# Performance work log

Hardware: AMD Instinct MI355X
Metric: run time of the kernel (lower is better)

## Reference

```python
import jax, jax.numpy as jnp
import numpy as np

D_MODEL = 1024
NUM_HEADS = 16
HEAD_DIM = D_MODEL // NUM_HEADS


def setup_inputs() -> dict:
    key = jax.random.key(0)
    ks = jax.random.split(key, 10)
    B, SQ, SK = 2, 2048, 2048
    scale = 1.0 / np.sqrt(D_MODEL)
    inp = {
        "x1": jax.random.normal(ks[0], (B, SQ, D_MODEL), jnp.float32),
        "x2": jax.random.normal(ks[1], (B, SK, D_MODEL), jnp.float32),
        "Wq": jax.random.normal(ks[2], (D_MODEL, D_MODEL), jnp.float32) * scale,
        "bq": jnp.zeros((D_MODEL,), jnp.float32),
        "Wk": jax.random.normal(ks[3], (D_MODEL, D_MODEL), jnp.float32) * scale,
        "bk": jnp.zeros((D_MODEL,), jnp.float32),
        "Wv": jax.random.normal(ks[4], (D_MODEL, D_MODEL), jnp.float32) * scale,
        "bv": jnp.zeros((D_MODEL,), jnp.float32),
        "Wo": jax.random.normal(ks[5], (D_MODEL, D_MODEL), jnp.float32) * scale,
        "bo": jnp.zeros((D_MODEL,), jnp.float32),
    }
    return inp


def reference(x1, x2, Wq, bq, Wk, bk, Wv, bv, Wo, bo):
    B, SQ, _ = x1.shape
    SK = x2.shape[1]
    # projections, then split into heads: [B, H, S, Dh]
    def split_heads(t, S):
        return t.reshape(B, S, NUM_HEADS, HEAD_DIM).transpose(0, 2, 1, 3)
    Q = split_heads(x1 @ Wq + bq, SQ)
    K = split_heads(x2 @ Wk + bk, SK)
    V = split_heads(x2 @ Wv + bv, SK)
    # note: original scales by 1/head_dim**0.5
    scores = jnp.einsum("bhqd,bhkd->bhqk", Q, K) / jnp.sqrt(
        jnp.asarray(HEAD_DIM, Q.dtype))
    attn = jax.nn.softmax(scores, axis=-1)
    ctx = jnp.einsum("bhqk,bhkd->bhqd", attn, V)
    ctx = ctx.transpose(0, 2, 1, 3).reshape(B, SQ, D_MODEL)
    return ctx @ Wo + bo
```

## Files before the change

kernel.cpp:

```cpp
#include <hip/hip_runtime.h>
#include <stdint.h>


typedef unsigned short u16b;
typedef __attribute__((ext_vector_type(4))) short short4v;
typedef __attribute__((ext_vector_type(8))) short short8v;
typedef __attribute__((ext_vector_type(4))) float float4v;
typedef __attribute__((ext_vector_type(2))) unsigned int uint2v;

#if __has_builtin(__builtin_amdgcn_exp2f)
__device__ __forceinline__ float exp2_fast(float x){ return __builtin_amdgcn_exp2f(x); }
#else
__device__ __forceinline__ float exp2_fast(float x){ return exp2f(x); }
#endif

__device__ __forceinline__ float bf2f(u16b u) {
  union { unsigned int i; float f; } v; v.i = ((unsigned int)u) << 16; return v.f;
}
__device__ __forceinline__ u16b f2bf(float f) {
  union { float f; unsigned int i; } v; v.f = f;
  return (u16b)((v.i + 0x7fffu + ((v.i >> 16) & 1u)) >> 16);
}
__device__ __forceinline__ void gl_lds16(const u16b* g, u16b* l) {
  __builtin_amdgcn_global_load_lds(
      (const __attribute__((address_space(1))) void*)g,
      (__attribute__((address_space(3))) void*)l, 16, 0, 0);
}

__global__ __launch_bounds__(256) void cvt2_bf16(
    const float* __restrict__ s0, const float* __restrict__ s1,
    u16b* __restrict__ d0, u16b* __restrict__ d1, int n4) {
  const float* src = blockIdx.y ? s1 : s0;
  u16b* dst = blockIdx.y ? d1 : d0;
  int i = blockIdx.x * blockDim.x + threadIdx.x;
  int stride = gridDim.x * blockDim.x;
  for (; i < n4; i += stride) {
    float4v v = ((const float4v*)src)[i];
    short4v o;
    o[0]=(short)f2bf(v[0]); o[1]=(short)f2bf(v[1]);
    o[2]=(short)f2bf(v[2]); o[3]=(short)f2bf(v[3]);
    ((short4v*)dst)[i] = o;
  }
}

__global__ __launch_bounds__(256) void transposeW(
    const float* __restrict__ W0, const float* __restrict__ W1,
    const float* __restrict__ W2, const float* __restrict__ W3,
    u16b* __restrict__ out) {
  __shared__ u16b tile[32][33];
  const int z = blockIdx.z;
  const float* src = (z==0) ? W0 : (z==1) ? W1 : (z==2) ? W2 : W3;
  u16b* dst = out + (size_t)z * (1024*1024);
  const int x = threadIdx.x, y = threadIdx.y;
  const int bx = blockIdx.x * 32, by = blockIdx.y * 32;
#pragma unroll
  for (int j=0;j<4;++j)
    tile[y*4+j][x] = f2bf(src[(size_t)(by + y*4+j)*1024 + bx + x]);
  __syncthreads();
#pragma unroll
  for (int j=0;j<4;++j)
    dst[(size_t)(bx + y*4+j)*1024 + by + x] = tile[x][y*4+j];
}

template<int BN, int OM>
__device__ __forceinline__ void gemm_core(
    const u16b* __restrict__ A, const u16b* __restrict__ Bt,
    const float* __restrict__ bias, void* __restrict__ Cv,
    int N, int K, int bm, int bn) {
  constexpr int NT = BN / 32;
  __shared__ __align__(16) u16b As[128*32];
  __shared__ __align__(16) u16b Bs[BN*32];
  const int tid = threadIdx.x;
  const int lane = tid & 63, wave = tid >> 6;
  const int wm = wave >> 1, wn = wave & 1;
  const int l15 = lane & 15, l4 = lane >> 4;
  float4v acc[4][NT];
#pragma unroll
  for (int i=0;i<4;++i)
#pragma unroll
    for (int j=0;j<NT;++j) acc[i][j] = (float4v){0.f,0.f,0.f,0.f};

  const int swz = (l15 >> 1) & 3;

  for (int k0 = 0; k0 < K; k0 += 32) {
    __syncthreads();
    {
      int row = tid >> 2, seg = tid & 3;
      int segg0 = seg ^ ((row >> 1) & 3);
      int row2 = row + 64;
      int segg1 = seg ^ ((row2 >> 1) & 3);
      gl_lds16(&A[(size_t)(bm+row )*K + k0 + segg0*8], &As[tid*8]);
      gl_lds16(&A[(size_t)(bm+row2)*K + k0 + segg1*8], &As[(tid+256)*8]);
      gl_lds16(&Bt[(size_t)(bn+row )*K + k0 + segg0*8], &Bs[tid*8]);
      if (BN == 128)
        gl_lds16(&Bt[(size_t)(bn+row2)*K + k0 + segg1*8], &Bs[(tid+256)*8]);
    }
    __syncthreads();
    short8v af[4], bf[NT];
#pragma unroll
    for (int mt=0;mt<4;++mt)
      af[mt] = *(const short8v*)&As[(wm*64+mt*16+l15)*32 + ((l4 ^ swz)*8)];
#pragma unroll
    for (int nt=0;nt<NT;++nt)
      bf[nt] = *(const short8v*)&Bs[(wn*(BN/2)+nt*16+l15)*32 + ((l4 ^ swz)*8)];
#pragma unroll
    for (int mt=0;mt<4;++mt)
#pragma unroll
      for (int nt=0;nt<NT;++nt)
        acc[mt][nt] = __builtin_amdgcn_mfma_f32_16x16x32_bf16(af[mt], bf[nt], acc[mt][nt], 0, 0, 0);
  }

#pragma unroll
  for (int nt=0;nt<NT;++nt) {
    int col = bn + wn*(BN/2) + nt*16 + l15;
    float bb = bias[col];
#pragma unroll
    for (int mt=0;mt<4;++mt) {
      int row0 = bm + wm*64 + mt*16 + l4*4;
      if (OM == 2) {
        int bloc = row0 >> 11, kv0 = row0 & 2047;
        uint2v dw;
        dw[0] = (unsigned)f2bf(acc[mt][nt][0] + bb) | ((unsigned)f2bf(acc[mt][nt][1] + bb) << 16);
        dw[1] = (unsigned)f2bf(acc[mt][nt][2] + bb) | ((unsigned)f2bf(acc[mt][nt][3] + bb) << 16);
        *(uint2v*)((u16b*)Cv + ((size_t)(bloc*1024 + col))*2048 + kv0) = dw;
      } else {
#pragma unroll
        for (int r=0;r<4;++r) {
          float v = acc[mt][nt][r] + bb;
          if (OM == 1) ((float*)Cv)[(size_t)(row0+r)*N + col] = v;
          else         ((u16b*)Cv)[(size_t)(row0+r)*N + col] = f2bf(v);
        }
      }
    }
  }
}

__global__ __launch_bounds__(256) void gemm_qkv(
    const u16b* __restrict__ x1b, const u16b* __restrict__ x2b,
    const u16b* __restrict__ WT, const float* __restrict__ bq,
    const float* __restrict__ bk, const float* __restrict__ bv,
    u16b* __restrict__ out) {
  const int z = blockIdx.z;
  const u16b* A = (z == 0) ? x1b : x2b;
  const u16b* Bt = WT + (size_t)z * (1024*1024);
  u16b* C = out + (size_t)z * (4u*1024*1024);
  if (z == 2)
    gemm_core<128,2>(A, Bt, bv, C, 1024, 1024, blockIdx.y*128, blockIdx.x*128);
  else
    gemm_core<128,0>(A, Bt, (z==0)?bq:bk, C, 1024, 1024, blockIdx.y*128, blockIdx.x*128);
}

__global__ __launch_bounds__(256) void gemm_out(
    const u16b* __restrict__ A, const u16b* __restrict__ Bt,
    const float* __restrict__ bias, float* __restrict__ C) {
  gemm_core<64,1>(A, Bt, bias, C, 1024, 1024, blockIdx.y*128, blockIdx.x*64);
}

__global__ __launch_bounds__(256) void attn128(
    const u16b* __restrict__ Q, const u16b* __restrict__ Kg,
    const u16b* __restrict__ Vt, u16b* __restrict__ O) {
  __shared__ __align__(16) u16b Ks[128*64];
  __shared__ __align__(16) u16b Vs[64*128];
  __shared__ __align__(16) u16b Ps[4*2*16*72];
  const int tid = threadIdx.x;
  const int lane = tid & 63, wave = tid >> 6;
  const int l15 = lane & 15, l4 = lane >> 4;
  const int h = blockIdx.y, b = blockIdx.z;
  const int q0 = blockIdx.x * 128;
  const size_t seqbase = (size_t)b * 2048;
  const int colh = h * 64;
  const int vtbase = (b*16 + h) * 64;
  u16b* Pw = Ps + wave * 2304;

  const float qscale = 0.125f * 1.4426950408889634f;
  short8v qf[2][2];
#pragma unroll
  for (int g=0; g<2; ++g) {
    size_t qrow = seqbase + q0 + wave*32 + g*16 + l15;
#pragma unroll
    for (int ks=0; ks<2; ++ks) {
      short8v raw = *(const short8v*)&Q[qrow*1024 + colh + ks*32 + l4*8];
      short8v s;
#pragma unroll
      for (int i=0;i<8;++i) s[i] = (short)f2bf(bf2f((u16b)raw[i]) * qscale);
      qf[g][ks] = s;
    }
  }

  float lpart[2] = {0.f, 0.f};
  float4v oacc[2][4];
#pragma unroll
  for (int g=0; g<2; ++g)
#pragma unroll
    for (int nb=0; nb<4; ++nb) oacc[g][nb] = (float4v){0.f,0.f,0.f,0.f};

  for (int kt = 0; kt < 16; ++kt) {
    const size_t kvbase = seqbase + (size_t)kt*128;
    __syncthreads();
#pragma unroll
    for (int j=0; j<4; ++j) {
      int idx = j*256 + tid;
      {
        int row = idx >> 3, seg = idx & 7;
        gl_lds16(&Kg[(kvbase+row)*1024 + colh + ((seg ^ (row & 7))*8)], &Ks[idx*8]);
      }
      {
        int row = idx >> 4, seg = idx & 15;
        gl_lds16(&Vt[(size_t)(vtbase+row)*2048 + (size_t)kt*128 + ((seg ^ (row & 15))*8)],
                 &Vs[idx*8]);
      }
    }
    __syncthreads();

    float4v sacc[2][8];
#pragma unroll
    for (int g=0; g<2; ++g)
#pragma unroll
      for (int nb=0; nb<8; ++nb) sacc[g][nb] = (float4v){0.f,0.f,0.f,0.f};
#pragma unroll
    for (int nb=0; nb<8; ++nb)
#pragma unroll
      for (int ks=0; ks<2; ++ks) {
        short8v kf = *(const short8v*)&Ks[(nb*16+l15)*64 + (((ks*4+l4) ^ (l15 & 7))*8)];
        sacc[0][nb] = __builtin_amdgcn_mfma_f32_16x16x32_bf16(kf, qf[0][ks], sacc[0][nb], 0, 0, 0);
        sacc[1][nb] = __builtin_amdgcn_mfma_f32_16x16x32_bf16(kf, qf[1][ks], sacc[1][nb], 0, 0, 0);
      }

#pragma unroll
    for (int h2=0; h2<2; ++h2) {
#pragma unroll
      for (int g=0; g<2; ++g) {
        float ls = 0.f;
#pragma unroll
        for (int nbl=0; nbl<4; ++nbl) {
          const float4v s4 = sacc[g][h2*4 + nbl];
          unsigned int u0 = __float_as_uint(exp2_fast(s4[0]));
          unsigned int u1 = __float_as_uint(exp2_fast(s4[1]));
          unsigned int u2 = __float_as_uint(exp2_fast(s4[2]));
          unsigned int u3 = __float_as_uint(exp2_fast(s4[3]));
          ls += __uint_as_float(u0 & 0xFFFF0000u) + __uint_as_float(u1 & 0xFFFF0000u)
              + __uint_as_float(u2 & 0xFFFF0000u) + __uint_as_float(u3 & 0xFFFF0000u);
          uint2v dw;
          dw[0] = (u0 >> 16) | (u1 & 0xFFFF0000u);
          dw[1] = (u2 >> 16) | (u3 & 0xFFFF0000u);
          *(uint2v*)&Pw[g*1152 + l15*72 + nbl*16 + l4*4] = dw;
        }
        lpart[g] += ls;
      }
      __asm__ __volatile__("s_waitcnt lgkmcnt(0)" ::: "memory");

#pragma unroll
      for (int ks2=0; ks2<2; ++ks2) {
        short8v pf0 = *(const short8v*)&Pw[       l15*72 + ks2*32 + l4*8];
        short8v pf1 = *(const short8v*)&Pw[1152 + l15*72 + ks2*32 + l4*8];
#pragma unroll
        for (int nb=0; nb<4; ++nb) {
          int cc = (h2*8 + ks2*4 + l4) ^ l15;
          short8v vf = *(const short8v*)&Vs[(nb*16+l15)*128 + cc*8];
          oacc[0][nb] = __builtin_amdgcn_mfma_f32_16x16x32_bf16(pf0, vf, oacc[0][nb], 0, 0, 0);
          oacc[1][nb] = __builtin_amdgcn_mfma_f32_16x16x32_bf16(pf1, vf, oacc[1][nb], 0, 0, 0);
        }
      }
    }
  }

#pragma unroll
  for (int g=0; g<2; ++g) {
    float l = lpart[g];
    l += __shfl_xor(l, 16);
    l += __shfl_xor(l, 32);
#pragma unroll
    for (int r=0; r<4; ++r) {
      float ld = __shfl(l, (lane & 48) | (l4*4 + r), 64);
      float inv = 1.0f / ld;
      size_t row = seqbase + q0 + wave*32 + g*16 + l4*4 + r;
#pragma unroll
      for (int nb=0; nb<4; ++nb)
        O[row*1024 + colh + nb*16 + l15] = f2bf(oacc[g][nb][r] * inv);
    }
  }
}

extern "C" void kernel_launch(void* const* d_in, const int* in_sizes, int n_in,
                              void* d_out, int out_size, void* d_ws, size_t ws_size,
                              hipStream_t stream) {
  const float* x1 = (const float*)d_in[0];
  const float* x2 = (const float*)d_in[1];
  const float* Wq = (const float*)d_in[2];
  const float* bq = (const float*)d_in[3];
  const float* Wk = (const float*)d_in[4];
  const float* bk = (const float*)d_in[5];
  const float* Wv = (const float*)d_in[6];
  const float* bv = (const float*)d_in[7];
  const float* Wo = (const float*)d_in[8];
  const float* bo = (const float*)d_in[9];
  (void)in_sizes; (void)n_in; (void)out_size; (void)ws_size;

  u16b* ws = (u16b*)d_ws;
  const size_t Mi = 1024*1024;
  u16b* WT  = ws;
  u16b* WoT = ws + 3*Mi;
  u16b* x1b = ws + 4*Mi;
  u16b* x2b = ws + 8*Mi;
  u16b* QKV = ws + 12*Mi;
  u16b* Qb  = QKV;
  u16b* Kb  = QKV + 4*Mi;
  u16b* Vtb = QKV + 8*Mi;
  u16b* Cx  = x1b;

  cvt2_bf16<<<dim3(1024,2), 256, 0, stream>>>(x1, x2, x1b, x2b, (int)Mi);
  transposeW<<<dim3(32,32,4), dim3(32,8,1), 0, stream>>>(Wq, Wk, Wv, Wo, WT);

  gemm_qkv<<<dim3(8,32,3), 256, 0, stream>>>(x1b, x2b, WT, bq, bk, bv, QKV);

  attn128<<<dim3(16,16,2), 256, 0, stream>>>(Qb, Kb, Vtb, Cx);

  gemm_out<<<dim3(16,32), 256, 0, stream>>>(Cx, WoT, bo, (float*)d_out);
}
```

Measured before the change: 231.0 us.

## Halve attention query tile, compute row sums via MFMA, restructure V projection as transposed GEMM

The attention kernel now processes 64 query rows per block instead of 128, doubling the grid to raise occupancy and parallelism. The block index is ordered batch-head first, so consecutive blocks of one query tile cover different heads. Softmax row sums are accumulated with an extra MFMA against a ones vector instead of scalar adds and shuffles. The P buffer uses an XOR swizzle in place of padding. The V projection is computed as W^T·x^T with a row bias, producing a [1024 x 4096] transposed layout directly through the generic store path instead of a special packed store. The trade-off is that K/V tiles are reloaded twice as often per query row, and the V-projection stores become scalar bf16 writes.

```diff
diff --git a/kernel.cpp b/kernel.cpp
--- a/kernel.cpp
+++ b/kernel.cpp
@@ -62,14 +62,13 @@
     dst[(size_t)(bx + y*4+j)*1024 + by + x] = tile[x][y*4+j];
 }
 
-template<int BN, int OM>
+template<int BN, bool OUT_F32, bool BIAS_ROW>
 __device__ __forceinline__ void gemm_core(
+    u16b* __restrict__ As, u16b* __restrict__ Bs,
     const u16b* __restrict__ A, const u16b* __restrict__ Bt,
     const float* __restrict__ bias, void* __restrict__ Cv,
     int N, int K, int bm, int bn) {
   constexpr int NT = BN / 32;
-  __shared__ __align__(16) u16b As[128*32];
-  __shared__ __align__(16) u16b Bs[BN*32];
   const int tid = threadIdx.x;
   const int lane = tid & 63, wave = tid >> 6;
   const int wm = wave >> 1, wn = wave & 1;
@@ -113,23 +112,16 @@
 #pragma unroll
   for (int nt=0;nt<NT;++nt) {
     int col = bn + wn*(BN/2) + nt*16 + l15;
-    float bb = bias[col];
+    float bbc = BIAS_ROW ? 0.f : bias[col];
 #pragma unroll
     for (int mt=0;mt<4;++mt) {
       int row0 = bm + wm*64 + mt*16 + l4*4;
-      if (OM == 2) {
-        int bloc = row0 >> 11, kv0 = row0 & 2047;
-        uint2v dw;
-        dw[0] = (unsigned)f2bf(acc[mt][nt][0] + bb) | ((unsigned)f2bf(acc[mt][nt][1] + bb) << 16);
-        dw[1] = (unsigned)f2bf(acc[mt][nt][2] + bb) | ((unsigned)f2bf(acc[mt][nt][3] + bb) << 16);
-        *(uint2v*)((u16b*)Cv + ((size_t)(bloc*1024 + col))*2048 + kv0) = dw;
-      } else {
-#pragma unroll
-        for (int r=0;r<4;++r) {
-          float v = acc[mt][nt][r] + bb;
-          if (OM == 1) ((float*)Cv)[(size_t)(row0+r)*N + col] = v;
-          else         ((u16b*)Cv)[(size_t)(row0+r)*N + col] = f2bf(v);
-        }
+#pragma unroll
+      for (int r=0;r<4;++r) {
+        float bb = BIAS_ROW ? bias[row0+r] : bbc;
+        float v = acc[mt][nt][r] + bb;
+        if (OUT_F32) ((float*)Cv)[(size_t)(row0+r)*N + col] = v;
+        else         ((u16b*)Cv)[(size_t)(row0+r)*N + col] = f2bf(v);
       }
     }
   }
@@ -139,60 +131,68 @@
     const u16b* __restrict__ x1b, const u16b* __restrict__ x2b,
     const u16b* __restrict__ WT, const float* __restrict__ bq,
     const float* __restrict__ bk, const float* __restrict__ bv,
-    u16b* __restrict__ out) {
+    u16b* __restrict__ QKV) {
+  __shared__ __align__(16) u16b As[128*32];
+  __shared__ __align__(16) u16b Bs[128*32];
   const int z = blockIdx.z;
-  const u16b* A = (z == 0) ? x1b : x2b;
-  const u16b* Bt = WT + (size_t)z * (1024*1024);
-  u16b* C = out + (size_t)z * (4u*1024*1024);
-  if (z == 2)
-    gemm_core<128,2>(A, Bt, bv, C, 1024, 1024, blockIdx.y*128, blockIdx.x*128);
-  else
-    gemm_core<128,0>(A, Bt, (z==0)?bq:bk, C, 1024, 1024, blockIdx.y*128, blockIdx.x*128);
+  const size_t Mi = 1024*1024;
+  if (z == 2) {
+    gemm_core<128,false,true>(As, Bs, WT + 2*Mi, x2b, bv, QKV + 8*Mi,
+                              4096, 1024, blockIdx.x*128, blockIdx.y*128);
+  } else {
+    gemm_core<128,false,false>(As, Bs, z ? x2b : x1b, WT + (size_t)z*Mi,
+                               z ? bk : bq, QKV + (size_t)z*4*Mi,
+                               1024, 1024, blockIdx.y*128, blockIdx.x*128);
+  }
 }
 
 __global__ __launch_bounds__(256) void gemm_out(
     const u16b* __restrict__ A, const u16b* __restrict__ Bt,
     const float* __restrict__ bias, float* __restrict__ C) {
-  gemm_core<64,1>(A, Bt, bias, C, 1024, 1024, blockIdx.y*128, blockIdx.x*64);
-}
-
-__global__ __launch_bounds__(256) void attn128(
+  __shared__ __align__(16) u16b As[128*32];
+  __shared__ __align__(16) u16b Bs[64*32];
+  gemm_core<64,true,false>(As, Bs, A, Bt, bias, C, 1024, 1024,
+                           blockIdx.y*128, blockIdx.x*64);
+}
+
+__global__ __launch_bounds__(256) void attn_q64(
     const u16b* __restrict__ Q, const u16b* __restrict__ Kg,
     const u16b* __restrict__ Vt, u16b* __restrict__ O) {
   __shared__ __align__(16) u16b Ks[128*64];
   __shared__ __align__(16) u16b Vs[64*128];
-  __shared__ __align__(16) u16b Ps[4*2*16*72];
+  __shared__ __align__(16) u16b Ps[4*16*64];
   const int tid = threadIdx.x;
   const int lane = tid & 63, wave = tid >> 6;
   const int l15 = lane & 15, l4 = lane >> 4;
-  const int h = blockIdx.y, b = blockIdx.z;
-  const int q0 = blockIdx.x * 128;
+  const int bh = blockIdx.x;
+  const int b = bh >> 4, h = bh & 15;
+  const int q0 = blockIdx.y * 64;
   const size_t seqbase = (size_t)b * 2048;
   const int colh = h * 64;
-  const int vtbase = (b*16 + h) * 64;
-  u16b* Pw = Ps + wave * 2304;
+  u16b* Pw = Ps + wave * 1024;
 
   const float qscale = 0.125f * 1.4426950408889634f;
-  short8v qf[2][2];
-#pragma unroll
-  for (int g=0; g<2; ++g) {
-    size_t qrow = seqbase + q0 + wave*32 + g*16 + l15;
+  short8v qf[2];
+  {
+    size_t qrow = seqbase + q0 + wave*16 + l15;
 #pragma unroll
     for (int ks=0; ks<2; ++ks) {
       short8v raw = *(const short8v*)&Q[qrow*1024 + colh + ks*32 + l4*8];
       short8v s;
 #pragma unroll
       for (int i=0;i<8;++i) s[i] = (short)f2bf(bf2f((u16b)raw[i]) * qscale);
-      qf[g][ks] = s;
-    }
-  }
-
-  float lpart[2] = {0.f, 0.f};
-  float4v oacc[2][4];
-#pragma unroll
-  for (int g=0; g<2; ++g)
-#pragma unroll
-    for (int nb=0; nb<4; ++nb) oacc[g][nb] = (float4v){0.f,0.f,0.f,0.f};
+      qf[ks] = s;
+    }
+  }
+
+  short8v ones;
+#pragma unroll
+  for (int i=0;i<8;++i) ones[i] = (short)0x3F80;
+
+  float4v lacc = (float4v){0.f,0.f,0.f,0.f};
+  float4v oacc[4];
+#pragma unroll
+  for (int nb=0; nb<4; ++nb) oacc[nb] = (float4v){0.f,0.f,0.f,0.f};
 
   for (int kt = 0; kt < 16; ++kt) {
     const size_t kvbase = seqbase + (size_t)kt*128;
@@ -206,78 +206,66 @@
       }
       {
         int row = idx >> 4, seg = idx & 15;
-        gl_lds16(&Vt[(size_t)(vtbase+row)*2048 + (size_t)kt*128 + ((seg ^ (row & 15))*8)],
-                 &Vs[idx*8]);
+        gl_lds16(&Vt[(size_t)(h*64+row)*4096 + (size_t)b*2048 + kt*128
+                     + ((seg ^ (row & 15))*8)], &Vs[idx*8]);
       }
     }
     __syncthreads();
 
-    float4v sacc[2][8];
-#pragma unroll
-    for (int g=0; g<2; ++g)
-#pragma unroll
-      for (int nb=0; nb<8; ++nb) sacc[g][nb] = (float4v){0.f,0.f,0.f,0.f};
+    float4v sacc[8];
+#pragma unroll
+    for (int nb=0; nb<8; ++nb) sacc[nb] = (float4v){0.f,0.f,0.f,0.f};
 #pragma unroll
     for (int nb=0; nb<8; ++nb)
 #pragma unroll
       for (int ks=0; ks<2; ++ks) {
         short8v kf = *(const short8v*)&Ks[(nb*16+l15)*64 + (((ks*4+l4) ^ (l15 & 7))*8)];
-        sacc[0][nb] = __builtin_amdgcn_mfma_f32_16x16x32_bf16(kf, qf[0][ks], sacc[0][nb], 0, 0, 0);
-        sacc[1][nb] = __builtin_amdgcn_mfma_f32_16x16x32_bf16(kf, qf[1][ks], sacc[1][nb], 0, 0, 0);
+        sacc[nb] = __builtin_amdgcn_mfma_f32_16x16x32_bf16(kf, qf[ks], sacc[nb], 0, 0, 0);
       }
 
 #pragma unroll
     for (int h2=0; h2<2; ++h2) {
 #pragma unroll
-      for (int g=0; g<2; ++g) {
-        float ls = 0.f;
-#pragma unroll
-        for (int nbl=0; nbl<4; ++nbl) {
-          const float4v s4 = sacc[g][h2*4 + nbl];
-          unsigned int u0 = __float_as_uint(exp2_fast(s4[0]));
-          unsigned int u1 = __float_as_uint(exp2_fast(s4[1]));
-          unsigned int u2 = __float_as_uint(exp2_fast(s4[2]));
-          unsigned int u3 = __float_as_uint(exp2_fast(s4[3]));
-          ls += __uint_as_float(u0 & 0xFFFF0000u) + __uint_as_float(u1 & 0xFFFF0000u)
-              + __uint_as_float(u2 & 0xFFFF0000u) + __uint_as_float(u3 & 0xFFFF0000u);
-          uint2v dw;
-          dw[0] = (u0 >> 16) | (u1 & 0xFFFF0000u);
-          dw[1] = (u2 >> 16) | (u3 & 0xFFFF0000u);
-          *(uint2v*)&Pw[g*1152 + l15*72 + nbl*16 + l4*4] = dw;
-        }
-        lpart[g] += ls;
+      for (int nbl=0; nbl<4; ++nbl) {
+        const float4v s4 = sacc[h2*4 + nbl];
+        unsigned int u0 = __float_as_uint(exp2_fast(s4[0]));
+        unsigned int u1 = __float_as_uint(exp2_fast(s4[1]));
+        unsigned int u2 = __float_as_uint(exp2_fast(s4[2]));
+        unsigned int u3 = __float_as_uint(exp2_fast(s4[3]));
+        uint2v dw;
+        dw[0] = (u0 >> 16) | (u1 & 0xFFFF0000u);
+        dw[1] = (u2 >> 16) | (u3 & 0xFFFF0000u);
+        *(uint2v*)&Pw[l15*64 + (((nbl*4 + l4) ^ l15)*4)] = dw;
       }
       __asm__ __volatile__("s_waitcnt lgkmcnt(0)" ::: "memory");
 
 #pragma unroll
       for (int ks2=0; ks2<2; ++ks2) {
-        short8v pf0 = *(const short8v*)&Pw[       l15*72 + ks2*32 + l4*8];
-        short8v pf1 = *(const short8v*)&Pw[1152 + l15*72 + ks2*32 + l4*8];
+        int c0 = (ks2*8 + l4*2) ^ l15;
+        int c1 = (ks2*8 + l4*2 + 1) ^ l15;
+        short4v pa = *(const short4v*)&Pw[l15*64 + c0*4];
+        short4v pb = *(const short4v*)&Pw[l15*64 + c1*4];
+        short8v pf;
+        pf[0]=pa[0]; pf[1]=pa[1]; pf[2]=pa[2]; pf[3]=pa[3];
+        pf[4]=pb[0]; pf[5]=pb[1]; pf[6]=pb[2]; pf[7]=pb[3];
+        lacc = __builtin_amdgcn_mfma_f32_16x16x32_bf16(pf, ones, lacc, 0, 0, 0);
 #pragma unroll
         for (int nb=0; nb<4; ++nb) {
           int cc = (h2*8 + ks2*4 + l4) ^ l15;
           short8v vf = *(const short8v*)&Vs[(nb*16+l15)*128 + cc*8];
-          oacc[0][nb] = __builtin_amdgcn_mfma_f32_16x16x32_bf16(pf0, vf, oacc[0][nb], 0, 0, 0);
-          oacc[1][nb] = __builtin_amdgcn_mfma_f32_16x16x32_bf16(pf1, vf, oacc[1][nb], 0, 0, 0);
+          oacc[nb] = __builtin_amdgcn_mfma_f32_16x16x32_bf16(pf, vf, oacc[nb], 0, 0, 0);
         }
       }
     }
   }
 
 #pragma unroll
-  for (int g=0; g<2; ++g) {
-    float l = lpart[g];
-    l += __shfl_xor(l, 16);
-    l += __shfl_xor(l, 32);
-#pragma unroll
-    for (int r=0; r<4; ++r) {
-      float ld = __shfl(l, (lane & 48) | (l4*4 + r), 64);
-      float inv = 1.0f / ld;
-      size_t row = seqbase + q0 + wave*32 + g*16 + l4*4 + r;
-#pragma unroll
-      for (int nb=0; nb<4; ++nb)
-        O[row*1024 + colh + nb*16 + l15] = f2bf(oacc[g][nb][r] * inv);
-    }
+  for (int r=0; r<4; ++r) {
+    float inv = 1.0f / lacc[r];
+    size_t row = seqbase + q0 + wave*16 + l4*4 + r;
+#pragma unroll
+    for (int nb=0; nb<4; ++nb)
+      O[row*1024 + colh + nb*16 + l15] = f2bf(oacc[nb][r] * inv);
   }
 }
 
@@ -313,7 +301,7 @@
 
   gemm_qkv<<<dim3(8,32,3), 256, 0, stream>>>(x1b, x2b, WT, bq, bk, bv, QKV);
 
-  attn128<<<dim3(16,16,2), 256, 0, stream>>>(Qb, Kb, Vtb, Cx);
+  attn_q64<<<dim3(32,32), 256, 0, stream>>>(Qb, Kb, Vtb, Cx);
 
   gemm_out<<<dim3(16,32), 256, 0, stream>>>(Cx, WoT, bo, (float*)d_out);
 }
```

Measured after the change: 227.7 us. No clear change (-1.4%).
